# Performance work log

Measured on AMD Instinct MI355X. Metric: run time of the kernel, lower is better.

## Reference

```python
import jax, jax.numpy as jnp
import numpy as np

B, N, M, E, H = 8, 4096, 4, 512, 8
HEAD_DIM = E // H
LN_EPS = 1e-5


def setup_inputs() -> dict:
    key = jax.random.key(0)
    ks = jax.random.split(key, 12)
    inp = {}
    for i in range(M):
        inp[f"f{i}"] = jax.random.normal(ks[i], (B, N, E), dtype=jnp.float32)
    # learned query (flattened from [1,1,E])
    inp["q_param"] = jax.random.normal(ks[4], (E,), dtype=jnp.float32)
    # torch nn.MultiheadAttention packed in-projection [3E, E] and bias [3E]
    inp["in_proj_w"] = jax.random.normal(ks[5], (3 * E, E), dtype=jnp.float32) * 0.02
    inp["in_proj_b"] = jnp.zeros((3 * E,), dtype=jnp.float32)
    inp["out_proj_w"] = jax.random.normal(ks[6], (E, E), dtype=jnp.float32) * 0.02
    inp["out_proj_b"] = jnp.zeros((E,), dtype=jnp.float32)
    inp["ln_gamma"] = jnp.ones((E,), dtype=jnp.float32)
    inp["ln_beta"] = jnp.zeros((E,), dtype=jnp.float32)
    return inp


def reference(f0, f1, f2, f3, q_param, in_proj_w, in_proj_b, out_proj_w, out_proj_b, ln_gamma, ln_beta):
    x = jnp.stack([f0, f1, f2, f3], axis=2)  # [B, N, M, E]
    b, n, m, e = x.shape
    h, d = H, e // H
    scale = 1.0 / np.sqrt(d)

    Wq, Wk, Wv = jnp.split(in_proj_w, 3, axis=0)  # each [E, E]
    bq, bk, bv = jnp.split(in_proj_b, 3)

    # single learned query, shared across all (b, n) instances
    qh = ((Wq @ q_param + bq) * scale).reshape(h, d)  # [H, d]

    k = (jnp.einsum('bnme,fe->bnmf', x, Wk) + bk).reshape(b, n, m, h, d)
    v = (jnp.einsum('bnme,fe->bnmf', x, Wv) + bv).reshape(b, n, m, h, d)

    scores = jnp.einsum('hd,bnmhd->bnhm', qh, k)        # [B, N, H, M]
    attn = jax.nn.softmax(scores, axis=-1)
    o = jnp.einsum('bnhm,bnmhd->bnhd', attn, v).reshape(b, n, e)
    o = o @ out_proj_w.T + out_proj_b                   # [B, N, E]

    mu = jnp.mean(o, axis=-1, keepdims=True)
    var = jnp.var(o, axis=-1, keepdims=True)
    return (o - mu) * jax.lax.rsqrt(var + LN_EPS) * ln_gamma + ln_beta
```

## Files before the change

kernel.cpp:

```cpp
#include <hip/hip_runtime.h>
#include <hip/hip_bf16.h>


typedef float  f32x4  __attribute__((ext_vector_type(4)));
typedef float  f32x16 __attribute__((ext_vector_type(16)));
typedef short  short8 __attribute__((ext_vector_type(8)));
typedef unsigned int u32x2 __attribute__((ext_vector_type(2)));

__device__ __forceinline__ unsigned short f2bf(float f) {
  unsigned int x = __float_as_uint(f);
  unsigned int r = (x + 0x7fffu + ((x >> 16) & 1u)) >> 16;
  return (unsigned short)r;
}

__device__ __forceinline__ short8 pack8(const f32x4& a, const f32x4& b) {
  unsigned int r0, r1, r2, r3;
  asm("v_cvt_pk_bf16_f32 %0, %1, %2" : "=v"(r0) : "v"(a[0]), "v"(a[1]));
  asm("v_cvt_pk_bf16_f32 %0, %1, %2" : "=v"(r1) : "v"(a[2]), "v"(a[3]));
  asm("v_cvt_pk_bf16_f32 %0, %1, %2" : "=v"(r2) : "v"(b[0]), "v"(b[1]));
  asm("v_cvt_pk_bf16_f32 %0, %1, %2" : "=v"(r3) : "v"(b[2]), "v"(b[3]));
  short8 r;
  r[0] = (short)(r0 & 0xffff); r[1] = (short)(r0 >> 16);
  r[2] = (short)(r1 & 0xffff); r[3] = (short)(r1 >> 16);
  r[4] = (short)(r2 & 0xffff); r[5] = (short)(r2 >> 16);
  r[6] = (short)(r3 & 0xffff); r[7] = (short)(r3 >> 16);
  return r;
}

__device__ __forceinline__ u32x2 pack4(const f32x4& a) {
  u32x2 r;
  asm("v_cvt_pk_bf16_f32 %0, %1, %2" : "=v"(r[0]) : "v"(a[0]), "v"(a[1]));
  asm("v_cvt_pk_bf16_f32 %0, %1, %2" : "=v"(r[1]) : "v"(a[2]), "v"(a[3]));
  return r;
}

__device__ __forceinline__ void mfma32(f32x16& c, short8 a, short8 b) {
  asm("v_mfma_f32_32x32x16_bf16 %0, %1, %2, %0" : "+v"(c) : "v"(a), "v"(b));
}
__device__ __forceinline__ void mfma16(f32x4& c, short8 a, short8 b) {
  asm("v_mfma_f32_16x16x32_bf16 %0, %1, %2, %0" : "+v"(c) : "v"(a), "v"(b));
}

__device__ __forceinline__ void gld4f(f32x4& d, const float* p) {
  asm volatile("global_load_dwordx4 %0, %1, off" : "=v"(d) : "v"(p));
}
__device__ __forceinline__ void gld4s(short8& d, const unsigned short* p) {
  asm volatile("global_load_dwordx4 %0, %1, off" : "=v"(d) : "v"(p));
}

__device__ __forceinline__ void wxv4(f32x4& a, f32x4& b, f32x4& c, f32x4& d) {
  asm volatile("s_waitcnt vmcnt(4)" : "+v"(a), "+v"(b), "+v"(c), "+v"(d));
}
__device__ __forceinline__ void wxv8(f32x4& a, f32x4& b, f32x4& c, f32x4& d) {
  asm volatile("s_waitcnt vmcnt(8)" : "+v"(a), "+v"(b), "+v"(c), "+v"(d));
}
__device__ __forceinline__ void wxv12(f32x4& a, f32x4& b, f32x4& c, f32x4& d) {
  asm volatile("s_waitcnt vmcnt(12)" : "+v"(a), "+v"(b), "+v"(c), "+v"(d));
}
__device__ __forceinline__ void wbv4(short8& a, short8& b, short8& c, short8& d,
                                     short8& e, short8& f, short8& g, short8& h) {
  asm volatile("s_waitcnt vmcnt(4)"
               : "+v"(a), "+v"(b), "+v"(c), "+v"(d),
                 "+v"(e), "+v"(f), "+v"(g), "+v"(h));
}
__device__ __forceinline__ void wbv0(short8& a, short8& b, short8& c, short8& d,
                                     short8& e, short8& f, short8& g, short8& h) {
  asm volatile("s_waitcnt vmcnt(0)"
               : "+v"(a), "+v"(b), "+v"(c), "+v"(d),
                 "+v"(e), "+v"(f), "+v"(g), "+v"(h));
}

__global__ void __launch_bounds__(512) tdcp_k0(
    const float* __restrict__ q_param, const float* __restrict__ in_w,
    const float* __restrict__ in_b, const float* __restrict__ out_w,
    float* __restrict__ scoreb, unsigned short* __restrict__ wscB,
    unsigned short* __restrict__ WvB, unsigned short* __restrict__ WoB)
{
  const int tid = threadIdx.x;
  const int blk = blockIdx.x;
  if (blk < 8) {
    const int h = blk;
    __shared__ float qls[512];
    __shared__ float qs[64];
    qls[tid] = q_param[tid];
    __syncthreads();
    {
      const int io = tid >> 3, sub = tid & 7;
      const float* wrow = in_w + (size_t)(h * 64 + io) * 512;
      float v = 0.f;
      #pragma unroll 8
      for (int ee = 0; ee < 64; ++ee) {
        const int e = sub + (ee << 3);
        v += wrow[e] * qls[e];
      }
      v += __shfl_xor(v, 1); v += __shfl_xor(v, 2); v += __shfl_xor(v, 4);
      if (sub == 0) qs[io] = (v + in_b[h * 64 + io]) * 0.125f;
    }
    __syncthreads();
    {
      const int e = tid;
      const float* wk = in_w + (size_t)(512 + h * 64) * 512 + e;
      float v = 0.f;
      #pragma unroll 8
      for (int jj = 0; jj < 64; ++jj) v += qs[jj] * wk[jj * 512];
      const int s32 = e >> 5, g = (e & 31) >> 3, j = e & 7;
      wscB[((s32 << 6) + h + (g << 4)) * 8 + j] = f2bf(v);
      wscB[((s32 << 6) + (h + 8) + (g << 4)) * 8 + j] = 0;
    }
    if (tid < 64) {
      float v = qs[tid] * in_b[512 + h * 64 + tid];
      v += __shfl_xor(v, 1);  v += __shfl_xor(v, 2);  v += __shfl_xor(v, 4);
      v += __shfl_xor(v, 8);  v += __shfl_xor(v, 16); v += __shfl_xor(v, 32);
      if (tid == 0) scoreb[h] = v;
    }
    if (blk == 0 && tid >= 64 && tid < 72) scoreb[tid - 56] = 0.f;
  } else {
    const int mb = blk - 8;
    const bool isWo = mb >= 64;
    const float* src = isWo ? out_w : (in_w + (size_t)1024 * 512);
    unsigned short* dst = isWo ? WoB : WvB;
    const int slot = ((mb & 63) << 9) + tid;
    const int ct = slot >> 11, kt = (slot >> 6) & 31, ln = slot & 63;
    const float* p = src + (size_t)(ct * 32 + (ln & 31)) * 512
                         + kt * 16 + ((ln >> 5) << 3);
    const f32x4 u0 = *(const f32x4*)(p);
    const f32x4 u1 = *(const f32x4*)(p + 4);
    short8 rr;
    rr[0] = (short)f2bf(u0[0]); rr[1] = (short)f2bf(u0[1]);
    rr[2] = (short)f2bf(u0[2]); rr[3] = (short)f2bf(u0[3]);
    rr[4] = (short)f2bf(u1[0]); rr[5] = (short)f2bf(u1[1]);
    rr[6] = (short)f2bf(u1[2]); rr[7] = (short)f2bf(u1[3]);
    *(short8*)(dst + slot * 8) = rr;
  }
}

__global__ void __launch_bounds__(512, 2) tdcp_k1(
    const float* __restrict__ f0, const float* __restrict__ f1,
    const float* __restrict__ f2, const float* __restrict__ f3,
    const float* __restrict__ in_b,
    const float* __restrict__ scoreb, const unsigned short* __restrict__ wscB,
    const unsigned short* __restrict__ WvB, const unsigned short* __restrict__ WoB,
    const float* __restrict__ out_b, const float* __restrict__ gamma,
    const float* __restrict__ beta, float* __restrict__ out)
{
  __shared__ __align__(16) char smem[65536];
  const int tid = threadIdx.x;
  const int w = tid >> 6;
  const int l = tid & 63;
  const int tok0 = blockIdx.x << 5;

  {
    const f32x4* wsrc = (const f32x4*)wscB;
    f32x4* wdst = (f32x4*)(smem + 49152);
    wdst[tid * 2] = wsrc[tid * 2];
    wdst[tid * 2 + 1] = wsrc[tid * 2 + 1];
  }

  const int sr = tid >> 2;
  const int c = tid & 3;
  const int sm = sr & 3;
  const int stk = sr >> 2;
  const float* fsrc = (sm == 0 ? f0 : sm == 1 ? f1 : sm == 2 ? f2 : f3)
                      + (size_t)(tok0 + stk) * 512 + (c << 2);
  int wj[4];
  #pragma unroll
  for (int j = 0; j < 4; ++j)
    wj[j] = (j << 12) + ((sr >> 5) << 10) + ((c >> 1) << 9)
          + ((((sr & 31) << 4)) ^ (j << 5)) + ((c & 1) << 3);

  const int aO = ((l >> 5) << 9) + ((l & 31) << 4);
  const int sBase = ((w >> 1) << 10) + (((l >> 4) & 1) << 9)
                  + ((((w & 1) << 4) | (l & 15)) << 4);
  const int ct0 = w << 1;
  const unsigned short* wv0 = WvB + (((ct0 * 32) << 6) + l) * 8;
  const unsigned short* wv1 = WvB + ((((ct0 + 1) * 32) << 6) + l) * 8;
  const unsigned short* wscL = (const unsigned short*)(smem + 49152);

  f32x16 acc[4][2];
  f32x4 sacc;
  #pragma unroll
  for (int i = 0; i < 4; ++i)
    #pragma unroll
    for (int cc = 0; cc < 2; ++cc)
      #pragma unroll
      for (int r = 0; r < 16; ++r) acc[i][cc][r] = 0.f;
  sacc[0] = sacc[1] = sacc[2] = sacc[3] = 0.f;

  f32x4 lx[2][4];
  short8 bb[2][8];

  gld4f(lx[0][0], fsrc);      gld4f(lx[0][1], fsrc + 16);
  gld4f(lx[0][2], fsrc + 32); gld4f(lx[0][3], fsrc + 48);
  gld4f(lx[1][0], fsrc + 64); gld4f(lx[1][1], fsrc + 80);
  gld4f(lx[1][2], fsrc + 96); gld4f(lx[1][3], fsrc + 112);
  wxv4(lx[0][0], lx[0][1], lx[0][2], lx[0][3]);
  #pragma unroll
  for (int j = 0; j < 4; ++j)
    *(u32x2*)(smem + wj[j]) = pack4(lx[0][j]);
  #pragma unroll
  for (int j = 0; j < 4; ++j) {
    gld4s(bb[0][2 * j],     wv0 + j * 512);
    gld4s(bb[0][2 * j + 1], wv1 + j * 512);
  }
  gld4f(lx[0][0], fsrc + 128); gld4f(lx[0][1], fsrc + 144);
  gld4f(lx[0][2], fsrc + 160); gld4f(lx[0][3], fsrc + 176);
  asm volatile("s_waitcnt lgkmcnt(0)" ::: "memory");
  __builtin_amdgcn_s_barrier();
  asm volatile("" ::: "memory");

  #pragma unroll
  for (int s = 0; s < 8; ++s) {
    if (s < 7) {
      f32x4 (&L)[4] = lx[(s + 1) & 1];
      if (s < 6) wxv12(L[0], L[1], L[2], L[3]);
      else       wxv8(L[0], L[1], L[2], L[3]);
      char* nb = smem + 16384 * ((s + 1) % 3);
      #pragma unroll
      for (int j = 0; j < 4; ++j)
        *(u32x2*)(nb + wj[j]) = pack4(L[j]);
    }
    asm volatile("s_waitcnt lgkmcnt(0)" ::: "memory");
    __builtin_amdgcn_s_barrier();
    asm volatile("" ::: "memory");

    short8 (&b)[8] = bb[s & 1];
    if (s < 6) wbv4(b[0], b[1], b[2], b[3], b[4], b[5], b[6], b[7]);
    else       wbv0(b[0], b[1], b[2], b[3], b[4], b[5], b[6], b[7]);
    char* cur = smem + 16384 * (s % 3);
    const short8 sb0 = *(const short8*)(wscL + (((2 * s) << 6) + l) * 8);
    const short8 sb1 = *(const short8*)(wscL + (((2 * s + 1) << 6) + l) * 8);
    #pragma unroll
    for (int kt4 = 0; kt4 < 4; ++kt4) {
      #pragma unroll
      for (int rt = 0; rt < 4; ++rt) {
        const short8 a = *(const short8*)(cur + (kt4 << 12) + (rt << 10)
                                          + (aO ^ (kt4 << 5)));
        mfma32(acc[rt][0], a, b[kt4 * 2]);
        mfma32(acc[rt][1], a, b[kt4 * 2 + 1]);
      }
      if ((kt4 & 1) == 0) {
        const int schunk = kt4 + (l >> 5);
        const short8 sa = *(const short8*)(cur + (schunk << 12)
                                           + (sBase ^ ((schunk & 3) << 5)));
        mfma16(sacc, sa, (kt4 == 0) ? sb0 : sb1);
      }
    }
    if (s < 7) {
      short8 (&nbf)[8] = bb[(s + 1) & 1];
      #pragma unroll
      for (int j = 0; j < 4; ++j) {
        gld4s(nbf[2 * j],     wv0 + ((s + 1) * 4 + j) * 512);
        gld4s(nbf[2 * j + 1], wv1 + ((s + 1) * 4 + j) * 512);
      }
    }
    if (s < 5) {
      f32x4 (&L)[4] = lx[(s + 3) & 1];
      const float* p = fsrc + ((s + 3) << 6);
      gld4f(L[0], p); gld4f(L[1], p + 16); gld4f(L[2], p + 32); gld4f(L[3], p + 48);
    }
  }
  asm volatile("s_nop 7\n\ts_nop 7\n\ts_nop 7" ::);

  {
    const int hh = l & 15;
    if (hh < 8) {
      const float sb = scoreb[hh];
      const float s0 = sacc[0] + sb, s1 = sacc[1] + sb;
      const float s2 = sacc[2] + sb, s3 = sacc[3] + sb;
      const float mx = fmaxf(fmaxf(s0, s1), fmaxf(s2, s3));
      const float e0 = __expf(s0 - mx), e1 = __expf(s1 - mx);
      const float e2 = __expf(s2 - mx), e3 = __expf(s3 - mx);
      const float inv = 1.f / (e0 + e1 + e2 + e3);
      f32x4 av; av[0] = e0 * inv; av[1] = e1 * inv; av[2] = e2 * inv; av[3] = e3 * inv;
      const int t = (w << 2) + (l >> 4);
      *(f32x4*)(smem + 32768 + (((t << 3) + hh) << 4)) = av;
    }
  }
  __syncthreads();

  {
    unsigned short* omid = (unsigned short*)(smem);
    #pragma unroll
    for (int c2 = 0; c2 < 2; ++c2) {
      const int ff = ((ct0 + c2) << 5) + (l & 31);
      const float bvf = in_b[1024 + ff];
      const int ktf = ff >> 4;
      const int laneL = ((l >> 3) & 1) << 5;
      const int elem = ff & 7;
      #pragma unroll
      for (int rt = 0; rt < 4; ++rt) {
        #pragma unroll
        for (int tt = 0; tt < 4; ++tt) {
          const int t = (rt << 3) + (tt << 1) + (l >> 5);
          const f32x4 av = *(const f32x4*)(smem + 32768 + (((t << 3) + w) << 4));
          const float o = av[0] * acc[rt][c2][tt * 4 + 0]
                        + av[1] * acc[rt][c2][tt * 4 + 1]
                        + av[2] * acc[rt][c2][tt * 4 + 2]
                        + av[3] * acc[rt][c2][tt * 4 + 3] + bvf;
          omid[((ktf << 6) + t + laneL) * 8 + elem] = f2bf(o);
        }
      }
    }
  }
  __syncthreads();

  f32x16 oa0, oa1;
  #pragma unroll
  for (int r = 0; r < 16; ++r) { oa0[r] = 0.f; oa1[r] = 0.f; }
  const unsigned short* wo0 = WoB + (((ct0 * 32) << 6) + l) * 8;
  const unsigned short* wo1 = WoB + ((((ct0 + 1) * 32) << 6) + l) * 8;
  const int a_off = l << 4;
  #pragma unroll 4
  for (int kt = 0; kt < 32; ++kt) {
    const short8 a = *(const short8*)(smem + (kt << 10) + a_off);
    mfma32(oa0, a, *(const short8*)(wo0 + kt * 512));
    mfma32(oa1, a, *(const short8*)(wo1 + kt * 512));
  }
  asm volatile("s_nop 7\n\ts_nop 7\n\ts_nop 7" ::);

  {
    const int g0 = (ct0 << 5) + (l & 31);
    const int g1 = g0 + 32;
    const float ob0 = out_b[g0], ob1 = out_b[g1];
    const float gm0 = gamma[g0], gm1 = gamma[g1];
    const float bt0 = beta[g0],  bt1 = beta[g1];
    float* stats = (float*)(smem + 36864);
    #pragma unroll
    for (int r = 0; r < 16; ++r) {
      const float v0 = oa0[r] + ob0, v1 = oa1[r] + ob1;
      float s = v0 + v1, qq = v0 * v0 + v1 * v1;
      s += __shfl_xor(s, 16); qq += __shfl_xor(qq, 16);
      s += __shfl_xor(s, 8);  qq += __shfl_xor(qq, 8);
      s += __shfl_xor(s, 4);  qq += __shfl_xor(qq, 4);
      s += __shfl_xor(s, 2);  qq += __shfl_xor(qq, 2);
      s += __shfl_xor(s, 1);  qq += __shfl_xor(qq, 1);
      if ((l & 31) == 0) {
        const int t = (r & 3) + ((r >> 2) << 3) + ((l >> 5) << 2);
        stats[(t << 4) + (w << 1)] = s;
        stats[(t << 4) + (w << 1) + 1] = qq;
      }
    }
    __syncthreads();
    #pragma unroll
    for (int r = 0; r < 16; ++r) {
      const int t = (r & 3) + ((r >> 2) << 3) + ((l >> 5) << 2);
      const float* st = stats + (t << 4);
      float s = 0.f, qq = 0.f;
      #pragma unroll
      for (int ww = 0; ww < 8; ++ww) { s += st[2 * ww]; qq += st[2 * ww + 1]; }
      const float mu = s * 0.001953125f;
      const float rs = rsqrtf(qq * 0.001953125f - mu * mu + 1e-5f);
      const float v0 = oa0[r] + ob0, v1 = oa1[r] + ob1;
      float* op = out + (size_t)(tok0 + t) * 512;
      op[g0] = (v0 - mu) * rs * gm0 + bt0;
      op[g1] = (v1 - mu) * rs * gm1 + bt1;
    }
  }
}

extern "C" void kernel_launch(void* const* d_in, const int* in_sizes, int n_in,
                              void* d_out, int out_size, void* d_ws, size_t ws_size,
                              hipStream_t stream) {
  const float* f0      = (const float*)d_in[0];
  const float* f1      = (const float*)d_in[1];
  const float* f2      = (const float*)d_in[2];
  const float* f3      = (const float*)d_in[3];
  const float* q_param = (const float*)d_in[4];
  const float* in_w    = (const float*)d_in[5];
  const float* in_b    = (const float*)d_in[6];
  const float* out_w   = (const float*)d_in[7];
  const float* out_b   = (const float*)d_in[8];
  const float* gamma   = (const float*)d_in[9];
  const float* beta    = (const float*)d_in[10];
  float* out = (float*)d_out;

  char* ws = (char*)d_ws;
  float* scoreb          = (float*)ws;
  unsigned short* wscB   = (unsigned short*)(ws + 4096);
  unsigned short* WvB    = (unsigned short*)(ws + 20480);
  unsigned short* WoB    = (unsigned short*)(ws + 544768);

  tdcp_k0<<<136, 512, 0, stream>>>(q_param, in_w, in_b, out_w,
                                   scoreb, wscB, WvB, WoB);
  tdcp_k1<<<1024, 512, 0, stream>>>(f0, f1, f2, f3, in_b,
                                    scoreb, wscB, WvB, WoB,
                                    out_b, gamma, beta, out);
}
```

Measured before the change: 149.0 us.

## Split fused score/V-projection loop into two phases with full bf16 tile staging

Restructures the main kernel so all eight bf16 input stages are written into a 128 KB LDS buffer while only the score MFMAs run, then performs the V-projection MFMAs in a second pass over the resident tiles. The score weights are now streamed from global memory instead of being staged in LDS. The aim is to cut per-stage barriers and let input loads overlap with a lighter loop. In exchange it uses 137 KB of dynamic shared memory per block, which drops occupancy from two blocks per CU to one, and it removes the overlap of input streaming with the heavy V-projection MFMAs.

```diff
diff --git a/kernel.cpp b/kernel.cpp
--- a/kernel.cpp
+++ b/kernel.cpp
@@ -11,20 +11,6 @@
   unsigned int x = __float_as_uint(f);
   unsigned int r = (x + 0x7fffu + ((x >> 16) & 1u)) >> 16;
   return (unsigned short)r;
-}
-
-__device__ __forceinline__ short8 pack8(const f32x4& a, const f32x4& b) {
-  unsigned int r0, r1, r2, r3;
-  asm("v_cvt_pk_bf16_f32 %0, %1, %2" : "=v"(r0) : "v"(a[0]), "v"(a[1]));
-  asm("v_cvt_pk_bf16_f32 %0, %1, %2" : "=v"(r1) : "v"(a[2]), "v"(a[3]));
-  asm("v_cvt_pk_bf16_f32 %0, %1, %2" : "=v"(r2) : "v"(b[0]), "v"(b[1]));
-  asm("v_cvt_pk_bf16_f32 %0, %1, %2" : "=v"(r3) : "v"(b[2]), "v"(b[3]));
-  short8 r;
-  r[0] = (short)(r0 & 0xffff); r[1] = (short)(r0 >> 16);
-  r[2] = (short)(r1 & 0xffff); r[3] = (short)(r1 >> 16);
-  r[4] = (short)(r2 & 0xffff); r[5] = (short)(r2 >> 16);
-  r[6] = (short)(r3 & 0xffff); r[7] = (short)(r3 >> 16);
-  return r;
 }
 
 __device__ __forceinline__ u32x2 pack4(const f32x4& a) {
@@ -48,18 +34,19 @@
   asm volatile("global_load_dwordx4 %0, %1, off" : "=v"(d) : "v"(p));
 }
 
-__device__ __forceinline__ void wxv4(f32x4& a, f32x4& b, f32x4& c, f32x4& d) {
-  asm volatile("s_waitcnt vmcnt(4)" : "+v"(a), "+v"(b), "+v"(c), "+v"(d));
-}
-__device__ __forceinline__ void wxv8(f32x4& a, f32x4& b, f32x4& c, f32x4& d) {
-  asm volatile("s_waitcnt vmcnt(8)" : "+v"(a), "+v"(b), "+v"(c), "+v"(d));
-}
-__device__ __forceinline__ void wxv12(f32x4& a, f32x4& b, f32x4& c, f32x4& d) {
-  asm volatile("s_waitcnt vmcnt(12)" : "+v"(a), "+v"(b), "+v"(c), "+v"(d));
-}
-__device__ __forceinline__ void wbv4(short8& a, short8& b, short8& c, short8& d,
+__device__ __forceinline__ void wA6(f32x4& a, f32x4& b, f32x4& c, f32x4& d,
+                                    short8& e, short8& f) {
+  asm volatile("s_waitcnt vmcnt(6)"
+               : "+v"(a), "+v"(b), "+v"(c), "+v"(d), "+v"(e), "+v"(f));
+}
+__device__ __forceinline__ void wA0(f32x4& a, f32x4& b, f32x4& c, f32x4& d,
+                                    short8& e, short8& f) {
+  asm volatile("s_waitcnt vmcnt(0)"
+               : "+v"(a), "+v"(b), "+v"(c), "+v"(d), "+v"(e), "+v"(f));
+}
+__device__ __forceinline__ void wbv8(short8& a, short8& b, short8& c, short8& d,
                                      short8& e, short8& f, short8& g, short8& h) {
-  asm volatile("s_waitcnt vmcnt(4)"
+  asm volatile("s_waitcnt vmcnt(8)"
                : "+v"(a), "+v"(b), "+v"(c), "+v"(d),
                  "+v"(e), "+v"(f), "+v"(g), "+v"(h));
 }
@@ -134,6 +121,9 @@
   }
 }
 
+#define AV_OFF 131072
+#define ST_OFF 135168
+
 __global__ void __launch_bounds__(512, 2) tdcp_k1(
     const float* __restrict__ f0, const float* __restrict__ f1,
     const float* __restrict__ f2, const float* __restrict__ f3,
@@ -143,18 +133,11 @@
     const float* __restrict__ out_b, const float* __restrict__ gamma,
     const float* __restrict__ beta, float* __restrict__ out)
 {
-  __shared__ __align__(16) char smem[65536];
+  extern __shared__ __align__(16) char smem[];
   const int tid = threadIdx.x;
   const int w = tid >> 6;
   const int l = tid & 63;
   const int tok0 = blockIdx.x << 5;
-
-  {
-    const f32x4* wsrc = (const f32x4*)wscB;
-    f32x4* wdst = (f32x4*)(smem + 49152);
-    wdst[tid * 2] = wsrc[tid * 2];
-    wdst[tid * 2 + 1] = wsrc[tid * 2 + 1];
-  }
 
   const int sr = tid >> 2;
   const int c = tid & 3;
@@ -174,91 +157,55 @@
   const int ct0 = w << 1;
   const unsigned short* wv0 = WvB + (((ct0 * 32) << 6) + l) * 8;
   const unsigned short* wv1 = WvB + ((((ct0 + 1) * 32) << 6) + l) * 8;
-  const unsigned short* wscL = (const unsigned short*)(smem + 49152);
-
-  f32x16 acc[4][2];
+
   f32x4 sacc;
-  #pragma unroll
-  for (int i = 0; i < 4; ++i)
-    #pragma unroll
-    for (int cc = 0; cc < 2; ++cc)
-      #pragma unroll
-      for (int r = 0; r < 16; ++r) acc[i][cc][r] = 0.f;
   sacc[0] = sacc[1] = sacc[2] = sacc[3] = 0.f;
 
   f32x4 lx[2][4];
-  short8 bb[2][8];
-
-  gld4f(lx[0][0], fsrc);      gld4f(lx[0][1], fsrc + 16);
-  gld4f(lx[0][2], fsrc + 32); gld4f(lx[0][3], fsrc + 48);
-  gld4f(lx[1][0], fsrc + 64); gld4f(lx[1][1], fsrc + 80);
-  gld4f(lx[1][2], fsrc + 96); gld4f(lx[1][3], fsrc + 112);
-  wxv4(lx[0][0], lx[0][1], lx[0][2], lx[0][3]);
-  #pragma unroll
-  for (int j = 0; j < 4; ++j)
-    *(u32x2*)(smem + wj[j]) = pack4(lx[0][j]);
-  #pragma unroll
-  for (int j = 0; j < 4; ++j) {
-    gld4s(bb[0][2 * j],     wv0 + j * 512);
-    gld4s(bb[0][2 * j + 1], wv1 + j * 512);
-  }
-  gld4f(lx[0][0], fsrc + 128); gld4f(lx[0][1], fsrc + 144);
-  gld4f(lx[0][2], fsrc + 160); gld4f(lx[0][3], fsrc + 176);
-  asm volatile("s_waitcnt lgkmcnt(0)" ::: "memory");
-  __builtin_amdgcn_s_barrier();
-  asm volatile("" ::: "memory");
-
-  #pragma unroll
-  for (int s = 0; s < 8; ++s) {
-    if (s < 7) {
-      f32x4 (&L)[4] = lx[(s + 1) & 1];
-      if (s < 6) wxv12(L[0], L[1], L[2], L[3]);
-      else       wxv8(L[0], L[1], L[2], L[3]);
-      char* nb = smem + 16384 * ((s + 1) % 3);
-      #pragma unroll
-      for (int j = 0; j < 4; ++j)
-        *(u32x2*)(nb + wj[j]) = pack4(L[j]);
-    }
-    asm volatile("s_waitcnt lgkmcnt(0)" ::: "memory");
-    __builtin_amdgcn_s_barrier();
-    asm volatile("" ::: "memory");
-
-    short8 (&b)[8] = bb[s & 1];
-    if (s < 6) wbv4(b[0], b[1], b[2], b[3], b[4], b[5], b[6], b[7]);
-    else       wbv0(b[0], b[1], b[2], b[3], b[4], b[5], b[6], b[7]);
-    char* cur = smem + 16384 * (s % 3);
-    const short8 sb0 = *(const short8*)(wscL + (((2 * s) << 6) + l) * 8);
-    const short8 sb1 = *(const short8*)(wscL + (((2 * s + 1) << 6) + l) * 8);
-    #pragma unroll
-    for (int kt4 = 0; kt4 < 4; ++kt4) {
-      #pragma unroll
-      for (int rt = 0; rt < 4; ++rt) {
-        const short8 a = *(const short8*)(cur + (kt4 << 12) + (rt << 10)
-                                          + (aO ^ (kt4 << 5)));
-        mfma32(acc[rt][0], a, b[kt4 * 2]);
-        mfma32(acc[rt][1], a, b[kt4 * 2 + 1]);
-      }
-      if ((kt4 & 1) == 0) {
-        const int schunk = kt4 + (l >> 5);
-        const short8 sa = *(const short8*)(cur + (schunk << 12)
-                                           + (sBase ^ ((schunk & 3) << 5)));
-        mfma16(sacc, sa, (kt4 == 0) ? sb0 : sb1);
-      }
-    }
-    if (s < 7) {
-      short8 (&nbf)[8] = bb[(s + 1) & 1];
-      #pragma unroll
-      for (int j = 0; j < 4; ++j) {
-        gld4s(nbf[2 * j],     wv0 + ((s + 1) * 4 + j) * 512);
-        gld4s(nbf[2 * j + 1], wv1 + ((s + 1) * 4 + j) * 512);
-      }
-    }
-    if (s < 5) {
-      f32x4 (&L)[4] = lx[(s + 3) & 1];
-      const float* p = fsrc + ((s + 3) << 6);
-      gld4f(L[0], p); gld4f(L[1], p + 16); gld4f(L[2], p + 32); gld4f(L[3], p + 48);
-    }
-  }
+  short8 sbb[2][2];
+
+#define ISSUE_L(S, bank) do {                                     \
+    const float* p_ = fsrc + ((S) << 6);                          \
+    gld4f(lx[bank][0], p_);      gld4f(lx[bank][1], p_ + 16);     \
+    gld4f(lx[bank][2], p_ + 32); gld4f(lx[bank][3], p_ + 48);     \
+  } while (0)
+
+#define ISSUE_SB(S, bank) do {                                    \
+    gld4s(sbb[bank][0], wscB + (((2 * (S)) << 6) + l) * 8);       \
+    gld4s(sbb[bank][1], wscB + (((2 * (S) + 1) << 6) + l) * 8);   \
+  } while (0)
+
+#define STEPA(S) do {                                                       \
+    const int bk_ = (S) & 1;                                                \
+    if ((S) < 7) wA6(lx[bk_][0], lx[bk_][1], lx[bk_][2], lx[bk_][3],        \
+                     sbb[bk_][0], sbb[bk_][1]);                             \
+    else         wA0(lx[bk_][0], lx[bk_][1], lx[bk_][2], lx[bk_][3],        \
+                     sbb[bk_][0], sbb[bk_][1]);                             \
+    char* nb_ = smem + 16384 * (S);                                         \
+    *(u32x2*)(nb_ + wj[0]) = pack4(lx[bk_][0]);                             \
+    *(u32x2*)(nb_ + wj[1]) = pack4(lx[bk_][1]);                             \
+    *(u32x2*)(nb_ + wj[2]) = pack4(lx[bk_][2]);                             \
+    *(u32x2*)(nb_ + wj[3]) = pack4(lx[bk_][3]);                             \
+    asm volatile("s_waitcnt lgkmcnt(0)" ::: "memory");                      \
+    {                                                                       \
+      const int sc0_ = 0 + (l >> 5);                                        \
+      const short8 sa0_ = *(const short8*)(nb_ + (sc0_ << 12)               \
+                                           + (sBase ^ ((sc0_ & 3) << 5)));  \
+      mfma16(sacc, sa0_, sbb[bk_][0]);                                      \
+      const int sc1_ = 2 + (l >> 5);                                        \
+      const short8 sa1_ = *(const short8*)(nb_ + (sc1_ << 12)               \
+                                           + (sBase ^ ((sc1_ & 3) << 5)));  \
+      mfma16(sacc, sa1_, sbb[bk_][1]);                                      \
+    }                                                                       \
+    if ((S) < 6) { ISSUE_L((S) + 2, bk_); ISSUE_SB((S) + 2, bk_); }         \
+  } while (0)
+
+  ISSUE_L(0, 0); ISSUE_SB(0, 0);
+  ISSUE_L(1, 1); ISSUE_SB(1, 1);
+
+  STEPA(0); STEPA(1); STEPA(2); STEPA(3);
+  STEPA(4); STEPA(5); STEPA(6); STEPA(7);
+
   asm volatile("s_nop 7\n\ts_nop 7\n\ts_nop 7" ::);
 
   {
@@ -273,9 +220,51 @@
       const float inv = 1.f / (e0 + e1 + e2 + e3);
       f32x4 av; av[0] = e0 * inv; av[1] = e1 * inv; av[2] = e2 * inv; av[3] = e3 * inv;
       const int t = (w << 2) + (l >> 4);
-      *(f32x4*)(smem + 32768 + (((t << 3) + hh) << 4)) = av;
-    }
-  }
+      *(f32x4*)(smem + AV_OFF + (((t << 3) + hh) << 4)) = av;
+    }
+  }
+  __syncthreads();
+
+  f32x16 acc[4][2];
+  #pragma unroll
+  for (int i = 0; i < 4; ++i)
+    #pragma unroll
+    for (int cc = 0; cc < 2; ++cc)
+      #pragma unroll
+      for (int r = 0; r < 16; ++r) acc[i][cc][r] = 0.f;
+
+  short8 bb[2][8];
+#define ISSUE_B(S, k) do { \
+    gld4s(bb[k][0], wv0 + ((S) * 4 + 0) * 512); \
+    gld4s(bb[k][1], wv1 + ((S) * 4 + 0) * 512); \
+    gld4s(bb[k][2], wv0 + ((S) * 4 + 1) * 512); \
+    gld4s(bb[k][3], wv1 + ((S) * 4 + 1) * 512); \
+    gld4s(bb[k][4], wv0 + ((S) * 4 + 2) * 512); \
+    gld4s(bb[k][5], wv1 + ((S) * 4 + 2) * 512); \
+    gld4s(bb[k][6], wv0 + ((S) * 4 + 3) * 512); \
+    gld4s(bb[k][7], wv1 + ((S) * 4 + 3) * 512); \
+  } while (0)
+
+  ISSUE_B(0, 0); ISSUE_B(1, 1);
+  #pragma unroll
+  for (int s = 0; s < 8; ++s) {
+    short8 (&b)[8] = bb[s & 1];
+    if (s < 7) wbv8(b[0], b[1], b[2], b[3], b[4], b[5], b[6], b[7]);
+    else       wbv0(b[0], b[1], b[2], b[3], b[4], b[5], b[6], b[7]);
+    const char* cur = smem + 16384 * s;
+    #pragma unroll
+    for (int kt4 = 0; kt4 < 4; ++kt4) {
+      #pragma unroll
+      for (int rt = 0; rt < 4; ++rt) {
+        const short8 a = *(const short8*)(cur + (kt4 << 12) + (rt << 10)
+                                          + (aO ^ (kt4 << 5)));
+        mfma32(acc[rt][0], a, b[kt4 * 2]);
+        mfma32(acc[rt][1], a, b[kt4 * 2 + 1]);
+      }
+    }
+    if (s < 6) ISSUE_B(s + 2, s & 1);
+  }
+  asm volatile("s_nop 7\n\ts_nop 7\n\ts_nop 7" ::);
   __syncthreads();
 
   {
@@ -292,7 +281,7 @@
         #pragma unroll
         for (int tt = 0; tt < 4; ++tt) {
           const int t = (rt << 3) + (tt << 1) + (l >> 5);
-          const f32x4 av = *(const f32x4*)(smem + 32768 + (((t << 3) + w) << 4));
+          const f32x4 av = *(const f32x4*)(smem + AV_OFF + (((t << 3) + w) << 4));
           const float o = av[0] * acc[rt][c2][tt * 4 + 0]
                         + av[1] * acc[rt][c2][tt * 4 + 1]
                         + av[2] * acc[rt][c2][tt * 4 + 2]
@@ -324,7 +313,7 @@
     const float ob0 = out_b[g0], ob1 = out_b[g1];
     const float gm0 = gamma[g0], gm1 = gamma[g1];
     const float bt0 = beta[g0],  bt1 = beta[g1];
-    float* stats = (float*)(smem + 36864);
+    float* stats = (float*)(smem + ST_OFF);
     #pragma unroll
     for (int r = 0; r < 16; ++r) {
       const float v0 = oa0[r] + ob0, v1 = oa1[r] + ob1;
@@ -344,7 +333,7 @@
     #pragma unroll
     for (int r = 0; r < 16; ++r) {
       const int t = (r & 3) + ((r >> 2) << 3) + ((l >> 5) << 2);
-      const float* st = stats + (t << 4);
+      const float* st = (const float*)(smem + ST_OFF) + (t << 4);
       float s = 0.f, qq = 0.f;
       #pragma unroll
       for (int ww = 0; ww < 8; ++ww) { s += st[2 * ww]; qq += st[2 * ww + 1]; }
@@ -356,6 +345,10 @@
       op[g1] = (v1 - mu) * rs * gm1 + bt1;
     }
   }
+#undef ISSUE_L
+#undef ISSUE_SB
+#undef STEPA
+#undef ISSUE_B
 }
 
 extern "C" void kernel_launch(void* const* d_in, const int* in_sizes, int n_in,
@@ -380,9 +373,12 @@
   unsigned short* WvB    = (unsigned short*)(ws + 20480);
   unsigned short* WoB    = (unsigned short*)(ws + 544768);
 
+  hipFuncSetAttribute((const void*)tdcp_k1,
+                      hipFuncAttributeMaxDynamicSharedMemorySize, 137216);
+
   tdcp_k0<<<136, 512, 0, stream>>>(q_param, in_w, in_b, out_w,
                                    scoreb, wscB, WvB, WoB);
-  tdcp_k1<<<1024, 512, 0, stream>>>(f0, f1, f2, f3, in_b,
-                                    scoreb, wscB, WvB, WoB,
-                                    out_b, gamma, beta, out);
-}
+  tdcp_k1<<<1024, 512, 137216, stream>>>(f0, f1, f2, f3, in_b,
+                                         scoreb, wscB, WvB, WoB,
+                                         out_b, gamma, beta, out);
+}
```

Measured after the change: 165.1 us. 10.8% more time.
